# Optimization experiments

Measured on AMD Instinct MI355X. Metric: run time of the kernel, lower is better.

The kernel has to match this reference:

```python
import jax, jax.numpy as jnp
import numpy as np
import math

B, S, H, D = 4, 4096, 2048, 128  # batch, seq_len, hidden_dim, head_size

def setup_inputs() -> dict:
    key = jax.random.key(0)
    ks = jax.random.split(key, 7)
    scale = 1.0 / math.sqrt(H)
    return {
        "x": jax.random.normal(ks[0], (B, S, H), dtype=jnp.float32),
        "Wq": jax.random.normal(ks[1], (H, D), dtype=jnp.float32) * scale,
        "bq": jnp.zeros((D,), dtype=jnp.float32),
        "Wk": jax.random.normal(ks[2], (H, D), dtype=jnp.float32) * scale,
        "bk": jnp.zeros((D,), dtype=jnp.float32),
        "Wv": jax.random.normal(ks[3], (H, D), dtype=jnp.float32) * scale,
        "bv": jnp.zeros((D,), dtype=jnp.float32),
    }

def reference(x, Wq, bq, Wk, bk, Wv, bv):
    # projections: [B,S,D]
    q = x @ Wq + bq
    k = x @ Wk + bk
    v = x @ Wv + bv
    # raw scores [B,S,S] with causal mask, NO pre-softmax scaling (as in source)
    scores = jnp.einsum('bsd,btd->bst', q, k)
    causal = jnp.tril(jnp.ones((S, S), dtype=bool))
    scores = jnp.where(causal, scores, -jnp.inf)
    # non-standard: scale AFTER softmax by 1/sqrt(head_size)
    w = jax.nn.softmax(scores, axis=-1) * (1.0 / math.sqrt(D))
    # dropout p=0.0 -> identity
    return jnp.einsum('bst,btd->bsd', w, v)
```

## Files before the change

kernel.cpp:

```cpp
#include <hip/hip_runtime.h>
#include <math.h>
#include <stdint.h>

#define SEQ   4096
#define HID   2048
#define HD    128
#define NROWS 16384

typedef __attribute__((ext_vector_type(8))) short bf16x8;
typedef __attribute__((ext_vector_type(4))) float f32x4;

static constexpr float OSCALE = 0.088388347648318447f;

using gvptr = const __attribute__((address_space(1))) void*;
using lvptr = __attribute__((address_space(3))) void*;
__device__ __forceinline__ void gld_lds16(const void* g, void* l) {
    __builtin_amdgcn_global_load_lds((gvptr)g, (lvptr)l, 16, 0, 0);
}

__device__ __forceinline__ unsigned short f2bf_rne(float f) {
    union { float f; unsigned u; } v; v.f = f;
    unsigned u = v.u + 0x7fffu + ((v.u >> 16) & 1u);
    return (unsigned short)(u >> 16);
}
__device__ __forceinline__ unsigned short f2bf_tr(float f) {
    union { float f; unsigned u; } v; v.f = f;
    return (unsigned short)(v.u >> 16);
}
__device__ __forceinline__ float bf2f(unsigned short h) {
    union { unsigned u; float f; } v; v.u = ((unsigned)h) << 16;
    return v.f;
}

__global__ __launch_bounds__(256) void prep_w(
    const float* __restrict__ Wq, const float* __restrict__ Wk, const float* __restrict__ Wv,
    unsigned short* __restrict__ wth, unsigned short* __restrict__ wtl)
{
    __shared__ float T[64][68];
    const int tid = threadIdx.x;
    const int k0 = blockIdx.x * 64, n0 = blockIdx.y * 64, mm = blockIdx.z;
    const float* W = (mm == 0) ? Wq : (mm == 1) ? Wk : Wv;
    #pragma unroll
    for (int i = 0; i < 4; ++i) {
        const int fi = i * 256 + tid, kk = fi >> 4, nc = (fi & 15) * 4;
        const float4 w = *(const float4*)(W + (size_t)(k0 + kk) * HD + n0 + nc);
        T[kk][nc] = w.x; T[kk][nc + 1] = w.y; T[kk][nc + 2] = w.z; T[kk][nc + 3] = w.w;
    }
    __syncthreads();
    unsigned short* oh = wth + (size_t)mm * HD * HID;
    unsigned short* ol = wtl + (size_t)mm * HD * HID;
    #pragma unroll
    for (int i = 0; i < 4; ++i) {
        const int fi = i * 256 + tid, nn = fi >> 4, kc = (fi & 15) * 4;
        const float a = T[kc][nn], b = T[kc + 1][nn], c = T[kc + 2][nn], d = T[kc + 3][nn];
        ushort4 hv, lv;
        hv.x = f2bf_rne(a); hv.y = f2bf_rne(b); hv.z = f2bf_rne(c); hv.w = f2bf_rne(d);
        lv.x = f2bf_rne(a - bf2f(hv.x)); lv.y = f2bf_rne(b - bf2f(hv.y));
        lv.z = f2bf_rne(c - bf2f(hv.z)); lv.w = f2bf_rne(d - bf2f(hv.w));
        *(ushort4*)(oh + (size_t)(n0 + nn) * HID + k0 + kc) = hv;
        *(ushort4*)(ol + (size_t)(n0 + nn) * HID + k0 + kc) = lv;
    }
}

__global__ __launch_bounds__(256, 2) void qkv_mfma(
    const float* __restrict__ x,
    const float* __restrict__ bq, const float* __restrict__ bk, const float* __restrict__ bv,
    const unsigned short* __restrict__ wth, const unsigned short* __restrict__ wtl,
    unsigned short* __restrict__ qh, unsigned short* __restrict__ ql,
    unsigned short* __restrict__ kh, unsigned short* __restrict__ kl,
    unsigned short* __restrict__ vth)
{
    __shared__ unsigned short Ah[128][40], Al[128][40];
    __shared__ unsigned short Bh[128][32], Bl[128][32];

    const int tid = threadIdx.x, wave = tid >> 6, lane = tid & 63;
    const int l15 = lane & 15, q4 = lane >> 4;
    const int wr = wave >> 1, wc = wave & 1;
    const int r0 = blockIdx.x * 128, mm = blockIdx.y;
    const int npass = (mm == 2) ? 1 : 3;
    const unsigned short* wt_h = wth + (size_t)mm * HD * HID;
    const unsigned short* wt_l = wtl + (size_t)mm * HD * HID;

    const int brow = lane >> 2;
    const int bsc  = ((lane & 3) ^ ((lane >> 3) & 3)) * 8;
    const int bkey = (l15 >> 1) & 3;

    f32x4 acc[4][4];
    #pragma unroll
    for (int i = 0; i < 4; ++i)
        #pragma unroll
        for (int j = 0; j < 4; ++j) acc[i][j] = (f32x4){0.f, 0.f, 0.f, 0.f};

    for (int k0 = 0; k0 < HID; k0 += 32) {
        float4 xv[4];
        #pragma unroll
        for (int i = 0; i < 4; ++i) {
            const int fi = i * 256 + tid, row = fi >> 3, kc = (fi & 7) * 4;
            xv[i] = *(const float4*)(x + (size_t)(r0 + row) * HID + k0 + kc);
        }
        __syncthreads();
        {
            const int rA = wave * 32 + brow, rB = rA + 16;
            gld_lds16(wt_h + (size_t)rA * HID + k0 + bsc, &Bh[wave * 32][0]);
            gld_lds16(wt_h + (size_t)rB * HID + k0 + bsc, &Bh[wave * 32 + 16][0]);
            if (npass == 3) {
                gld_lds16(wt_l + (size_t)rA * HID + k0 + bsc, &Bl[wave * 32][0]);
                gld_lds16(wt_l + (size_t)rB * HID + k0 + bsc, &Bl[wave * 32 + 16][0]);
            }
        }
        #pragma unroll
        for (int i = 0; i < 4; ++i) {
            const int fi = i * 256 + tid, row = fi >> 3, kc = (fi & 7) * 4;
            ushort4 hv, lv;
            hv.x = f2bf_tr(xv[i].x); hv.y = f2bf_tr(xv[i].y);
            hv.z = f2bf_tr(xv[i].z); hv.w = f2bf_tr(xv[i].w);
            *(ushort4*)&Ah[row][kc] = hv;
            if (npass == 3) {
                lv.x = f2bf_tr(xv[i].x - bf2f(hv.x)); lv.y = f2bf_tr(xv[i].y - bf2f(hv.y));
                lv.z = f2bf_tr(xv[i].z - bf2f(hv.z)); lv.w = f2bf_tr(xv[i].w - bf2f(hv.w));
                *(ushort4*)&Al[row][kc] = lv;
            }
        }
        __syncthreads();

        bf16x8 ah[4], bh_[4];
        #pragma unroll
        for (int t = 0; t < 4; ++t) {
            ah[t]  = *(const bf16x8*)&Ah[wr * 64 + t * 16 + l15][q4 * 8];
            bh_[t] = *(const bf16x8*)&Bh[wc * 64 + t * 16 + l15][(q4 ^ bkey) * 8];
        }
        if (npass == 3) {
            bf16x8 al[4], bl_[4];
            #pragma unroll
            for (int t = 0; t < 4; ++t) {
                al[t]  = *(const bf16x8*)&Al[wr * 64 + t * 16 + l15][q4 * 8];
                bl_[t] = *(const bf16x8*)&Bl[wc * 64 + t * 16 + l15][(q4 ^ bkey) * 8];
            }
            #pragma unroll
            for (int mt = 0; mt < 4; ++mt)
                #pragma unroll
                for (int nt = 0; nt < 4; ++nt) {
                    acc[mt][nt] = __builtin_amdgcn_mfma_f32_16x16x32_bf16(ah[mt], bh_[nt], acc[mt][nt], 0, 0, 0);
                    acc[mt][nt] = __builtin_amdgcn_mfma_f32_16x16x32_bf16(ah[mt], bl_[nt], acc[mt][nt], 0, 0, 0);
                    acc[mt][nt] = __builtin_amdgcn_mfma_f32_16x16x32_bf16(al[mt], bh_[nt], acc[mt][nt], 0, 0, 0);
                }
        } else {
            #pragma unroll
            for (int mt = 0; mt < 4; ++mt)
                #pragma unroll
                for (int nt = 0; nt < 4; ++nt)
                    acc[mt][nt] = __builtin_amdgcn_mfma_f32_16x16x32_bf16(ah[mt], bh_[nt], acc[mt][nt], 0, 0, 0);
        }
    }

    const float* bias = (mm == 0) ? bq : (mm == 1) ? bk : bv;
    if (mm < 2) {
        unsigned short* oh = (mm == 0) ? qh : kh;
        unsigned short* ol = (mm == 0) ? ql : kl;
        #pragma unroll
        for (int nt = 0; nt < 4; ++nt) {
            const int col = wc * 64 + nt * 16 + l15;
            const float bb = bias[col];
            #pragma unroll
            for (int mt = 0; mt < 4; ++mt) {
                const int Rb = r0 + wr * 64 + mt * 16 + q4 * 4;
                #pragma unroll
                for (int r = 0; r < 4; ++r) {
                    const float v = acc[mt][nt][r] + bb;
                    const unsigned short hh = f2bf_rne(v);
                    oh[(size_t)(Rb + r) * HD + col] = hh;
                    ol[(size_t)(Rb + r) * HD + col] = f2bf_rne(v - bf2f(hh));
                }
            }
        }
    } else {
        #pragma unroll
        for (int nt = 0; nt < 4; ++nt) {
            const int col = wc * 64 + nt * 16 + l15;
            const float bb = bias[col];
            #pragma unroll
            for (int mt = 0; mt < 4; ++mt) {
                const int Rb = r0 + wr * 64 + mt * 16 + q4 * 4;
                const int bi = Rb >> 12, s0 = Rb & 4095;
                ushort4 pv;
                pv.x = f2bf_rne(acc[mt][nt][0] + bb);
                pv.y = f2bf_rne(acc[mt][nt][1] + bb);
                pv.z = f2bf_rne(acc[mt][nt][2] + bb);
                pv.w = f2bf_rne(acc[mt][nt][3] + bb);
                *(ushort4*)(vth + ((size_t)(bi * HD + col)) * SEQ + s0) = pv;
            }
        }
    }
}

__global__ __launch_bounds__(256, 2) void flash_mfma(
    const unsigned short* __restrict__ qh, const unsigned short* __restrict__ ql,
    const unsigned short* __restrict__ kh, const unsigned short* __restrict__ kl,
    const unsigned short* __restrict__ vth,
    unsigned short* __restrict__ oPb, float* __restrict__ mP, float* __restrict__ lP)
{
    __shared__ unsigned short Kh[64][128], Kl[64][128];
    __shared__ unsigned short Vt[128][64];
    __shared__ unsigned short Ps[4][16][72];

    const int tid = threadIdx.x, wave = tid >> 6, lane = tid & 63;
    const int l15 = lane & 15, q4 = lane >> 4;
    const int h = blockIdx.x & 3, pair = (blockIdx.x >> 2) & 31, b = blockIdx.x >> 7;

    const int krow_l = lane >> 4;
    const int vrow_l = lane >> 3;
    const int vsc = ((lane & 7) ^ (vrow_l & 7)) * 8;
    const int kkey7 = l15 & 7;
    const int vkey7 = l15 & 7;

    for (int side = 0; side < 2; ++side) {
        const int tt = side ? (63 - pair) : pair;
        const int n = tt + 1;
        const int j0 = (n * h) >> 2, j1 = (n * (h + 1)) >> 2;

        const int qrow = b * SEQ + tt * 64 + wave * 16 + l15;
        bf16x8 aqh[4], aql[4];
        #pragma unroll
        for (int ks = 0; ks < 4; ++ks) {
            aqh[ks] = *(const bf16x8*)(qh + (size_t)qrow * HD + ks * 32 + q4 * 8);
            aql[ks] = *(const bf16x8*)(ql + (size_t)qrow * HD + ks * 32 + q4 * 8);
        }
        f32x4 oa[8];
        #pragma unroll
        for (int d = 0; d < 8; ++d) oa[d] = (f32x4){0.f, 0.f, 0.f, 0.f};
        float m_r[4] = {-INFINITY, -INFINITY, -INFINITY, -INFINITY};
        float l_r[4] = {0.f, 0.f, 0.f, 0.f};

        for (int j = j0; j < j1; ++j) {
            __syncthreads();
            {
                const size_t kb = (size_t)b * SEQ + j * 64;
                #pragma unroll
                for (int c = 0; c < 4; ++c) {
                    const int rl = c * 4 + krow_l;
                    const int sc = (l15 ^ (rl & 7)) * 8;
                    const size_t gr = (kb + wave * 16 + rl) * HD + sc;
                    gld_lds16(kh + gr, &Kh[wave * 16 + c * 4][0]);
                    gld_lds16(kl + gr, &Kl[wave * 16 + c * 4][0]);
                }
                #pragma unroll
                for (int c = 0; c < 4; ++c)
                    gld_lds16(vth + ((size_t)(b * HD + wave * 32 + c * 8 + vrow_l)) * SEQ
                                  + j * 64 + vsc,
                              &Vt[wave * 32 + c * 8][0]);
            }
            __syncthreads();

            f32x4 s[4];
            #pragma unroll
            for (int nt = 0; nt < 4; ++nt) s[nt] = (f32x4){0.f, 0.f, 0.f, 0.f};
            #pragma unroll
            for (int ks = 0; ks < 4; ++ks) {
                const int pc = ((ks * 4 + q4) ^ kkey7) * 8;
                #pragma unroll
                for (int nt = 0; nt < 4; ++nt) {
                    const bf16x8 bh = *(const bf16x8*)&Kh[nt * 16 + l15][pc];
                    const bf16x8 bl = *(const bf16x8*)&Kl[nt * 16 + l15][pc];
                    s[nt] = __builtin_amdgcn_mfma_f32_16x16x32_bf16(aqh[ks], bh, s[nt], 0, 0, 0);
                    s[nt] = __builtin_amdgcn_mfma_f32_16x16x32_bf16(aql[ks], bh, s[nt], 0, 0, 0);
                    s[nt] = __builtin_amdgcn_mfma_f32_16x16x32_bf16(aqh[ks], bl, s[nt], 0, 0, 0);
                }
            }
            if (j == tt) {
                #pragma unroll
                for (int nt = 0; nt < 4; ++nt) {
                    const int cl = nt * 16 + l15;
                    #pragma unroll
                    for (int r = 0; r < 4; ++r) {
                        const int rl = wave * 16 + q4 * 4 + r;
                        if (cl > rl) s[nt][r] = -INFINITY;
                    }
                }
            }
            #pragma unroll
            for (int r = 0; r < 4; ++r) {
                float mt = fmaxf(fmaxf(s[0][r], s[1][r]), fmaxf(s[2][r], s[3][r]));
                mt = fmaxf(mt, __shfl_xor(mt, 1));
                mt = fmaxf(mt, __shfl_xor(mt, 2));
                mt = fmaxf(mt, __shfl_xor(mt, 4));
                mt = fmaxf(mt, __shfl_xor(mt, 8));
                const float mn = fmaxf(m_r[r], mt);
                const float al = __expf(m_r[r] - mn);
                m_r[r] = mn;
                const float p0 = __expf(s[0][r] - mn), p1 = __expf(s[1][r] - mn);
                const float p2 = __expf(s[2][r] - mn), p3 = __expf(s[3][r] - mn);
                Ps[wave][q4 * 4 + r][l15]      = f2bf_tr(p0);
                Ps[wave][q4 * 4 + r][16 + l15] = f2bf_tr(p1);
                Ps[wave][q4 * 4 + r][32 + l15] = f2bf_tr(p2);
                Ps[wave][q4 * 4 + r][48 + l15] = f2bf_tr(p3);
                float ps = p0 + p1 + p2 + p3;
                ps += __shfl_xor(ps, 1); ps += __shfl_xor(ps, 2);
                ps += __shfl_xor(ps, 4); ps += __shfl_xor(ps, 8);
                l_r[r] = l_r[r] * al + ps;
                #pragma unroll
                for (int d = 0; d < 8; ++d) oa[d][r] *= al;
            }
            const bf16x8 ap0 = *(const bf16x8*)&Ps[wave][l15][q4 * 8];
            const bf16x8 ap1 = *(const bf16x8*)&Ps[wave][l15][32 + q4 * 8];
            #pragma unroll
            for (int d = 0; d < 8; ++d) {
                const bf16x8 bv0 = *(const bf16x8*)&Vt[d * 16 + l15][(q4 ^ vkey7) * 8];
                const bf16x8 bv1 = *(const bf16x8*)&Vt[d * 16 + l15][((4 + q4) ^ vkey7) * 8];
                oa[d] = __builtin_amdgcn_mfma_f32_16x16x32_bf16(ap0, bv0, oa[d], 0, 0, 0);
                oa[d] = __builtin_amdgcn_mfma_f32_16x16x32_bf16(ap1, bv1, oa[d], 0, 0, 0);
            }
        }

        const int R0 = b * SEQ + tt * 64 + wave * 16 + q4 * 4;
        unsigned short* op = oPb + (size_t)h * NROWS * HD;
        #pragma unroll
        for (int d = 0; d < 8; ++d)
            #pragma unroll
            for (int r = 0; r < 4; ++r)
                op[(size_t)(R0 + r) * HD + d * 16 + l15] = f2bf_rne(oa[d][r]);
        if (l15 == 0) {
            #pragma unroll
            for (int r = 0; r < 4; ++r) {
                mP[h * NROWS + R0 + r] = m_r[r];
                lP[h * NROWS + R0 + r] = l_r[r];
            }
        }
    }
}

__global__ __launch_bounds__(256) void flash_merge(
    const unsigned short* __restrict__ oPb, const float* __restrict__ mP,
    const float* __restrict__ lP, float* __restrict__ out)
{
    const int idx = blockIdx.x * 256 + threadIdx.x;
    const int r = idx >> 5, c = (idx & 31) * 4;
    float m[4], l[4];
    #pragma unroll
    for (int i = 0; i < 4; ++i) { m[i] = mP[i * NROWS + r]; l[i] = lP[i * NROWS + r]; }
    float M = fmaxf(fmaxf(m[0], m[1]), fmaxf(m[2], m[3]));
    float a[4], lsum = 0.f;
    #pragma unroll
    for (int i = 0; i < 4; ++i) { a[i] = __expf(m[i] - M); lsum += l[i] * a[i]; }
    const float inv = OSCALE / lsum;
    float ox = 0.f, oy = 0.f, oz = 0.f, ow = 0.f;
    #pragma unroll
    for (int i = 0; i < 4; ++i) {
        const ushort4 ov = *(const ushort4*)(oPb + (size_t)i * NROWS * HD + (size_t)r * HD + c);
        ox += a[i] * bf2f(ov.x); oy += a[i] * bf2f(ov.y);
        oz += a[i] * bf2f(ov.z); ow += a[i] * bf2f(ov.w);
    }
    float4 o; o.x = ox * inv; o.y = oy * inv; o.z = oz * inv; o.w = ow * inv;
    *(float4*)(out + (size_t)r * HD + c) = o;
}

extern "C" void kernel_launch(void* const* d_in, const int* in_sizes, int n_in,
                              void* d_out, int out_size, void* d_ws, size_t ws_size,
                              hipStream_t stream)
{
    (void)in_sizes; (void)n_in; (void)out_size; (void)ws_size;
    const float* x  = (const float*)d_in[0];
    const float* Wq = (const float*)d_in[1];
    const float* bq = (const float*)d_in[2];
    const float* Wk = (const float*)d_in[3];
    const float* bk = (const float*)d_in[4];
    const float* Wv = (const float*)d_in[5];
    const float* bv = (const float*)d_in[6];
    float* out = (float*)d_out;

    char* w = (char*)d_ws;
    unsigned short* qh  = (unsigned short*)(w);
    unsigned short* ql  = (unsigned short*)(w + 4194304);
    unsigned short* kh  = (unsigned short*)(w + 8388608);
    unsigned short* kl  = (unsigned short*)(w + 12582912);
    unsigned short* vth = (unsigned short*)(w + 16777216);
    unsigned short* wth = (unsigned short*)(w + 20971520);
    unsigned short* wtl = (unsigned short*)(w + 22544384);
    unsigned short* oPb = (unsigned short*)(w + 24117248);
    float* mP = (float*)(w + 40894464);
    float* lP = (float*)(w + 41156608);

    prep_w<<<dim3(32, 2, 3), 256, 0, stream>>>(Wq, Wk, Wv, wth, wtl);
    qkv_mfma<<<dim3(128, 3), 256, 0, stream>>>(x, bq, bk, bv, wth, wtl, qh, ql, kh, kl, vth);
    flash_mfma<<<512, 256, 0, stream>>>(qh, ql, kh, kl, vth, oPb, mP, lP);
    flash_merge<<<2048, 256, 0, stream>>>(oPb, mP, lP, out);
}
```

Measured before the change: 328.5 us.

## Fuse Q/K/V projections into one kernel sharing each x tile

The QKV projection now computes all three outputs in one block, so each x tile is loaded and split into bf16 hi/lo once instead of three times across separate Q, K and V blocks. Tiles shrink to 64 rows by 64 columns, the grid becomes 512 blocks, and launch bounds rise to 3 blocks per CU. The aim is less redundant global x traffic and conversion work. In exchange each block issues five weight-tile loads per step, and the smaller MFMA tiles give less operand reuse per LDS read.

```diff
diff --git a/kernel.cpp b/kernel.cpp
--- a/kernel.cpp
+++ b/kernel.cpp
@@ -62,7 +62,7 @@
     }
 }
 
-__global__ __launch_bounds__(256, 2) void qkv_mfma(
+__global__ __launch_bounds__(256, 3) void qkv_fused(
     const float* __restrict__ x,
     const float* __restrict__ bq, const float* __restrict__ bk, const float* __restrict__ bv,
     const unsigned short* __restrict__ wth, const unsigned short* __restrict__ wtl,
@@ -70,125 +70,121 @@
     unsigned short* __restrict__ kh, unsigned short* __restrict__ kl,
     unsigned short* __restrict__ vth)
 {
-    __shared__ unsigned short Ah[128][40], Al[128][40];
-    __shared__ unsigned short Bh[128][32], Bl[128][32];
+    __shared__ unsigned short Ah[64][40], Al[64][40];
+    __shared__ unsigned short Bt[5][64][32];
 
     const int tid = threadIdx.x, wave = tid >> 6, lane = tid & 63;
     const int l15 = lane & 15, q4 = lane >> 4;
     const int wr = wave >> 1, wc = wave & 1;
-    const int r0 = blockIdx.x * 128, mm = blockIdx.y;
-    const int npass = (mm == 2) ? 1 : 3;
-    const unsigned short* wt_h = wth + (size_t)mm * HD * HID;
-    const unsigned short* wt_l = wtl + (size_t)mm * HD * HID;
-
-    const int brow = lane >> 2;
-    const int bsc  = ((lane & 3) ^ ((lane >> 3) & 3)) * 8;
-    const int bkey = (l15 >> 1) & 3;
-
-    f32x4 acc[4][4];
-    #pragma unroll
-    for (int i = 0; i < 4; ++i)
-        #pragma unroll
-        for (int j = 0; j < 4; ++j) acc[i][j] = (f32x4){0.f, 0.f, 0.f, 0.f};
+    const int r0 = (blockIdx.x >> 1) * 64;
+    const int hc = blockIdx.x & 1;
+
+    const unsigned short* wsrc0 = wth + (size_t)hc * 64 * HID;
+    const unsigned short* wsrc1 = wtl + (size_t)hc * 64 * HID;
+    const unsigned short* wsrc2 = wth + (size_t)HD * HID + (size_t)hc * 64 * HID;
+    const unsigned short* wsrc3 = wtl + (size_t)HD * HID + (size_t)hc * 64 * HID;
+    const unsigned short* wsrc4 = wth + (size_t)2 * HD * HID + (size_t)hc * 64 * HID;
+
+    const int srow = wave * 16 + (lane >> 2);
+    const int schunk = ((lane & 3) ^ ((lane >> 2) & 3)) * 8;
+    const int pchunk = (q4 ^ (l15 & 3)) * 8;
+    const int bro = wc * 32;
+
+    f32x4 accq[2][2], acck[2][2], accv[2][2];
+    #pragma unroll
+    for (int i = 0; i < 2; ++i)
+        #pragma unroll
+        for (int j = 0; j < 2; ++j) {
+            accq[i][j] = (f32x4){0.f, 0.f, 0.f, 0.f};
+            acck[i][j] = (f32x4){0.f, 0.f, 0.f, 0.f};
+            accv[i][j] = (f32x4){0.f, 0.f, 0.f, 0.f};
+        }
 
     for (int k0 = 0; k0 < HID; k0 += 32) {
-        float4 xv[4];
-        #pragma unroll
-        for (int i = 0; i < 4; ++i) {
+        float4 xv[2];
+        #pragma unroll
+        for (int i = 0; i < 2; ++i) {
             const int fi = i * 256 + tid, row = fi >> 3, kc = (fi & 7) * 4;
             xv[i] = *(const float4*)(x + (size_t)(r0 + row) * HID + k0 + kc);
         }
         __syncthreads();
         {
-            const int rA = wave * 32 + brow, rB = rA + 16;
-            gld_lds16(wt_h + (size_t)rA * HID + k0 + bsc, &Bh[wave * 32][0]);
-            gld_lds16(wt_h + (size_t)rB * HID + k0 + bsc, &Bh[wave * 32 + 16][0]);
-            if (npass == 3) {
-                gld_lds16(wt_l + (size_t)rA * HID + k0 + bsc, &Bl[wave * 32][0]);
-                gld_lds16(wt_l + (size_t)rB * HID + k0 + bsc, &Bl[wave * 32 + 16][0]);
-            }
-        }
-        #pragma unroll
-        for (int i = 0; i < 4; ++i) {
+            gld_lds16(wsrc0 + (size_t)srow * HID + k0 + schunk, &Bt[0][wave * 16][0]);
+            gld_lds16(wsrc1 + (size_t)srow * HID + k0 + schunk, &Bt[1][wave * 16][0]);
+            gld_lds16(wsrc2 + (size_t)srow * HID + k0 + schunk, &Bt[2][wave * 16][0]);
+            gld_lds16(wsrc3 + (size_t)srow * HID + k0 + schunk, &Bt[3][wave * 16][0]);
+            gld_lds16(wsrc4 + (size_t)srow * HID + k0 + schunk, &Bt[4][wave * 16][0]);
+        }
+        #pragma unroll
+        for (int i = 0; i < 2; ++i) {
             const int fi = i * 256 + tid, row = fi >> 3, kc = (fi & 7) * 4;
             ushort4 hv, lv;
             hv.x = f2bf_tr(xv[i].x); hv.y = f2bf_tr(xv[i].y);
             hv.z = f2bf_tr(xv[i].z); hv.w = f2bf_tr(xv[i].w);
+            lv.x = f2bf_tr(xv[i].x - bf2f(hv.x)); lv.y = f2bf_tr(xv[i].y - bf2f(hv.y));
+            lv.z = f2bf_tr(xv[i].z - bf2f(hv.z)); lv.w = f2bf_tr(xv[i].w - bf2f(hv.w));
             *(ushort4*)&Ah[row][kc] = hv;
-            if (npass == 3) {
-                lv.x = f2bf_tr(xv[i].x - bf2f(hv.x)); lv.y = f2bf_tr(xv[i].y - bf2f(hv.y));
-                lv.z = f2bf_tr(xv[i].z - bf2f(hv.z)); lv.w = f2bf_tr(xv[i].w - bf2f(hv.w));
-                *(ushort4*)&Al[row][kc] = lv;
-            }
+            *(ushort4*)&Al[row][kc] = lv;
         }
         __syncthreads();
 
-        bf16x8 ah[4], bh_[4];
-        #pragma unroll
-        for (int t = 0; t < 4; ++t) {
-            ah[t]  = *(const bf16x8*)&Ah[wr * 64 + t * 16 + l15][q4 * 8];
-            bh_[t] = *(const bf16x8*)&Bh[wc * 64 + t * 16 + l15][(q4 ^ bkey) * 8];
-        }
-        if (npass == 3) {
-            bf16x8 al[4], bl_[4];
-            #pragma unroll
-            for (int t = 0; t < 4; ++t) {
-                al[t]  = *(const bf16x8*)&Al[wr * 64 + t * 16 + l15][q4 * 8];
-                bl_[t] = *(const bf16x8*)&Bl[wc * 64 + t * 16 + l15][(q4 ^ bkey) * 8];
-            }
-            #pragma unroll
-            for (int mt = 0; mt < 4; ++mt)
-                #pragma unroll
-                for (int nt = 0; nt < 4; ++nt) {
-                    acc[mt][nt] = __builtin_amdgcn_mfma_f32_16x16x32_bf16(ah[mt], bh_[nt], acc[mt][nt], 0, 0, 0);
-                    acc[mt][nt] = __builtin_amdgcn_mfma_f32_16x16x32_bf16(ah[mt], bl_[nt], acc[mt][nt], 0, 0, 0);
-                    acc[mt][nt] = __builtin_amdgcn_mfma_f32_16x16x32_bf16(al[mt], bh_[nt], acc[mt][nt], 0, 0, 0);
-                }
-        } else {
-            #pragma unroll
-            for (int mt = 0; mt < 4; ++mt)
-                #pragma unroll
-                for (int nt = 0; nt < 4; ++nt)
-                    acc[mt][nt] = __builtin_amdgcn_mfma_f32_16x16x32_bf16(ah[mt], bh_[nt], acc[mt][nt], 0, 0, 0);
-        }
-    }
-
-    const float* bias = (mm == 0) ? bq : (mm == 1) ? bk : bv;
-    if (mm < 2) {
-        unsigned short* oh = (mm == 0) ? qh : kh;
-        unsigned short* ol = (mm == 0) ? ql : kl;
-        #pragma unroll
-        for (int nt = 0; nt < 4; ++nt) {
-            const int col = wc * 64 + nt * 16 + l15;
-            const float bb = bias[col];
-            #pragma unroll
-            for (int mt = 0; mt < 4; ++mt) {
-                const int Rb = r0 + wr * 64 + mt * 16 + q4 * 4;
-                #pragma unroll
-                for (int r = 0; r < 4; ++r) {
-                    const float v = acc[mt][nt][r] + bb;
-                    const unsigned short hh = f2bf_rne(v);
-                    oh[(size_t)(Rb + r) * HD + col] = hh;
-                    ol[(size_t)(Rb + r) * HD + col] = f2bf_rne(v - bf2f(hh));
-                }
-            }
-        }
-    } else {
-        #pragma unroll
-        for (int nt = 0; nt < 4; ++nt) {
-            const int col = wc * 64 + nt * 16 + l15;
-            const float bb = bias[col];
-            #pragma unroll
-            for (int mt = 0; mt < 4; ++mt) {
-                const int Rb = r0 + wr * 64 + mt * 16 + q4 * 4;
-                const int bi = Rb >> 12, s0 = Rb & 4095;
-                ushort4 pv;
-                pv.x = f2bf_rne(acc[mt][nt][0] + bb);
-                pv.y = f2bf_rne(acc[mt][nt][1] + bb);
-                pv.z = f2bf_rne(acc[mt][nt][2] + bb);
-                pv.w = f2bf_rne(acc[mt][nt][3] + bb);
-                *(ushort4*)(vth + ((size_t)(bi * HD + col)) * SEQ + s0) = pv;
-            }
+        bf16x8 ah[2], al[2];
+        #pragma unroll
+        for (int mt = 0; mt < 2; ++mt) {
+            ah[mt] = *(const bf16x8*)&Ah[wr * 32 + mt * 16 + l15][q4 * 8];
+            al[mt] = *(const bf16x8*)&Al[wr * 32 + mt * 16 + l15][q4 * 8];
+        }
+        #pragma unroll
+        for (int nt = 0; nt < 2; ++nt) {
+            const int br = bro + nt * 16 + l15;
+            const bf16x8 qbh = *(const bf16x8*)&Bt[0][br][pchunk];
+            const bf16x8 qbl = *(const bf16x8*)&Bt[1][br][pchunk];
+            #pragma unroll
+            for (int mt = 0; mt < 2; ++mt) {
+                accq[mt][nt] = __builtin_amdgcn_mfma_f32_16x16x32_bf16(ah[mt], qbh, accq[mt][nt], 0, 0, 0);
+                accq[mt][nt] = __builtin_amdgcn_mfma_f32_16x16x32_bf16(ah[mt], qbl, accq[mt][nt], 0, 0, 0);
+                accq[mt][nt] = __builtin_amdgcn_mfma_f32_16x16x32_bf16(al[mt], qbh, accq[mt][nt], 0, 0, 0);
+            }
+            const bf16x8 kbh = *(const bf16x8*)&Bt[2][br][pchunk];
+            const bf16x8 kbl = *(const bf16x8*)&Bt[3][br][pchunk];
+            #pragma unroll
+            for (int mt = 0; mt < 2; ++mt) {
+                acck[mt][nt] = __builtin_amdgcn_mfma_f32_16x16x32_bf16(ah[mt], kbh, acck[mt][nt], 0, 0, 0);
+                acck[mt][nt] = __builtin_amdgcn_mfma_f32_16x16x32_bf16(ah[mt], kbl, acck[mt][nt], 0, 0, 0);
+                acck[mt][nt] = __builtin_amdgcn_mfma_f32_16x16x32_bf16(al[mt], kbh, acck[mt][nt], 0, 0, 0);
+            }
+            const bf16x8 vbh = *(const bf16x8*)&Bt[4][br][pchunk];
+            #pragma unroll
+            for (int mt = 0; mt < 2; ++mt)
+                accv[mt][nt] = __builtin_amdgcn_mfma_f32_16x16x32_bf16(ah[mt], vbh, accv[mt][nt], 0, 0, 0);
+        }
+    }
+
+    #pragma unroll
+    for (int nt = 0; nt < 2; ++nt) {
+        const int col = hc * 64 + wc * 32 + nt * 16 + l15;
+        const float bbq = bq[col], bbk = bk[col], bbv = bv[col];
+        #pragma unroll
+        for (int mt = 0; mt < 2; ++mt) {
+            const int Rb = r0 + wr * 32 + mt * 16 + q4 * 4;
+            #pragma unroll
+            for (int r = 0; r < 4; ++r) {
+                const float vq = accq[mt][nt][r] + bbq;
+                const unsigned short hq = f2bf_rne(vq);
+                qh[(size_t)(Rb + r) * HD + col] = hq;
+                ql[(size_t)(Rb + r) * HD + col] = f2bf_rne(vq - bf2f(hq));
+                const float vk = acck[mt][nt][r] + bbk;
+                const unsigned short hk = f2bf_rne(vk);
+                kh[(size_t)(Rb + r) * HD + col] = hk;
+                kl[(size_t)(Rb + r) * HD + col] = f2bf_rne(vk - bf2f(hk));
+            }
+            const int bi = Rb >> 12, s0 = Rb & 4095;
+            ushort4 pv;
+            pv.x = f2bf_rne(accv[mt][nt][0] + bbv);
+            pv.y = f2bf_rne(accv[mt][nt][1] + bbv);
+            pv.z = f2bf_rne(accv[mt][nt][2] + bbv);
+            pv.w = f2bf_rne(accv[mt][nt][3] + bbv);
+            *(ushort4*)(vth + ((size_t)(bi * HD + col)) * SEQ + s0) = pv;
         }
     }
 }
@@ -380,7 +376,7 @@
     float* lP = (float*)(w + 41156608);
 
     prep_w<<<dim3(32, 2, 3), 256, 0, stream>>>(Wq, Wk, Wv, wth, wtl);
-    qkv_mfma<<<dim3(128, 3), 256, 0, stream>>>(x, bq, bk, bv, wth, wtl, qh, ql, kh, kl, vth);
+    qkv_fused<<<512, 256, 0, stream>>>(x, bq, bk, bv, wth, wtl, qh, ql, kh, kl, vth);
     flash_mfma<<<512, 256, 0, stream>>>(qh, ql, kh, kl, vth, oPb, mP, lP);
     flash_merge<<<2048, 256, 0, stream>>>(oPb, mP, lP, out);
 }
```

Result: no change. 334.5 us (+1.8%).
